# Optimization experiments

Measured on AMD Instinct MI355X. Metric: run time of the kernel, lower is better.

The kernel has to match this reference:

```python
import jax, jax.numpy as jnp
from jax import lax
import numpy as np

B, S = 128, 512
TARGET_SIZE = 32
T = TARGET_SIZE + 4  # tag_size, START = T-2, END = T-1


def setup_inputs() -> dict:
    key = jax.random.key(0)
    k1, k2, k3, k4 = jax.random.split(key, 4)
    feats = jax.random.normal(k1, (B, S, T), dtype=jnp.float32)
    # contiguous-prefix mask (lengths in [S//2, S])
    lengths = jax.random.randint(k2, (B,), S // 2, S + 1)
    mask = (jnp.arange(S)[None, :] < lengths[:, None]).astype(jnp.int32)
    tags = jax.random.randint(k3, (B, S), 0, TARGET_SIZE).astype(jnp.int32)
    # learned transitions, with the hard constraints from __init__
    transitions = 0.1 * jax.random.normal(k4, (T, T), dtype=jnp.float32)
    transitions = transitions.at[:, T - 2].set(-1000.0)  # nothing -> START
    transitions = transitions.at[T - 1, :].set(-1000.0)  # END -> nothing
    return {"feats": feats, "transitions": transitions, "mask": mask, "tags": tags}


def _nll(feats, transitions, mask, tags):
    # feats: (B,S,T), transitions: (T,T) with [i,j] = score(prev=i -> cur=j)
    b, s, t = feats.shape
    START, END = t - 2, t - 1
    fdtype = feats.dtype

    feats_t = jnp.swapaxes(feats, 0, 1)   # (S,B,T)
    mask_t = jnp.swapaxes(mask, 0, 1)     # (S,B)

    # ---- forward algorithm (partition function) ----
    # scores[t,b,i,j] = feats[b,t,j] + transitions[i,j]
    part0 = feats_t[0] + transitions[START][None, :]  # (B,T): alpha after step 0

    def step(part, xs):
        f_step, m_step = xs  # (B,T), (B,)
        # cur[b,i,j] = feats[b,j] + trans[i,j] + part[b,i]
        cur = f_step[:, None, :] + transitions[None, :, :] + part[:, :, None]
        new_part = jax.nn.logsumexp(cur, axis=1)  # (B,T)
        part = jnp.where(m_step[:, None].astype(bool), new_part, part)
        return part, None

    part, _ = lax.scan(step, part0, (feats_t[1:], mask_t[1:]))
    final = jax.nn.logsumexp(part[:, :, None] + transitions[None, :, :], axis=1)  # (B,T)
    forward_score = jnp.sum(final[:, END])

    # ---- gold score ----
    tags_i = tags.astype(jnp.int32)
    prev_tags = jnp.concatenate(
        [jnp.full((b, 1), START, dtype=jnp.int32), tags_i[:, :-1]], axis=1)  # (B,S)
    emit = jnp.take_along_axis(feats, tags_i[:, :, None], axis=2)[:, :, 0]    # (B,S)
    trans_sc = transitions[prev_tags, tags_i]                                  # (B,S)
    tg_energy = jnp.sum((emit + trans_sc) * mask.astype(fdtype))
    lengths = jnp.sum(mask, axis=1).astype(jnp.int32)                          # (B,)
    end_ids = jnp.take_along_axis(tags_i, (lengths - 1)[:, None], axis=1)[:, 0]
    end_energy = jnp.sum(transitions[end_ids, END])
    gold_score = tg_energy + end_energy

    # average_batch = True
    return (forward_score - gold_score) / jnp.asarray(b, fdtype)


def reference(feats, transitions, mask, tags):
    return _nll(feats, transitions, mask, tags)
```

## Files before the change

### kernel.cpp

```cpp
#include <hip/hip_runtime.h>


namespace {
constexpr int kB = 128;
constexpr int kS = 512;
constexpr int kT = 36;
constexpr int kStart = 34;
constexpr int kEnd = 35;

__device__ __forceinline__ float readlane_f(float v, int lane) {
    return __builtin_bit_cast(float, __builtin_amdgcn_readlane(__builtin_bit_cast(int, v), lane));
}

__device__ __forceinline__ float wave_sum(float v) {
#pragma unroll
    for (int off = 32; off; off >>= 1) v += __shfl_xor(v, off, 64);
    return v;
}
__device__ __forceinline__ int wave_sum_i(int v) {
#pragma unroll
    for (int off = 32; off; off >>= 1) v += __shfl_xor(v, off, 64);
    return v;
}

#define FOR34(X) \
    X(0, 0) X(1, 1) X(2, 2) X(3, 3) X(4, 0) X(5, 1) X(6, 2) X(7, 3) \
    X(8, 0) X(9, 1) X(10, 2) X(11, 3) X(12, 0) X(13, 1) X(14, 2) X(15, 3) \
    X(16, 0) X(17, 1) X(18, 2) X(19, 3) X(20, 0) X(21, 1) X(22, 2) X(23, 3) \
    X(24, 0) X(25, 1) X(26, 2) X(27, 3) X(28, 0) X(29, 1) X(30, 2) X(31, 3) \
    X(32, 0) X(33, 1)

#define FMDECL(n, a) float Fm##n;
#define FMINIT(n, a) Fm##n = __expf(trans[(n)*kT + jc]);
#define BMDECL(n, a) float Bm##n;
#define BMINIT(n, a) Bm##n = __expf(trans[jc * kT + (n)]);
#define FDOT(n, a) v##a = fmaf(readlane_f(q, n), Fm##n, v##a);
#define BDOT(n, a) w##a = fmaf(readlane_f(pp, n), Bm##n, w##a);

#define LDT(t) fl[(size_t)(((t) < 0) ? 0 : (((t) > kS - 1) ? (kS - 1) : (t))) * kT]

__global__ __attribute__((amdgpu_flat_work_group_size(512, 512)))
void crf_seg_kernel(const float* __restrict__ feats,
                    const float* __restrict__ trans,
                    const int* __restrict__ mask,
                    const int* __restrict__ tags,
                    float* __restrict__ out) {
    const int b = blockIdx.x;
    const int tid = threadIdx.x;
    const int wv = tid >> 6;
    const int j = tid & 63;
    const int jc = (j < kT) ? j : (kT - 1);
    const float* fbase = feats + (size_t)b * kS * kT;
    const float* fl = fbase + jc;
    const int* mb = mask + b * kS;
    const int* tb = tags + b * kS;

    __shared__ float vec[8][64];
    __shared__ float cc[8];

    int len = 0;
#pragma unroll
    for (int k = 0; k < kS / 64; ++k) len += mb[k * 64 + j];
    len = __builtin_amdgcn_readfirstlane(wave_sum_i(len));

    const int c = (len + 3) / 5;
    const int Gp = (c + 3) >> 2;

    float C = 0.f;

    if (wv < 4) {
        FOR34(FMDECL)
        FOR34(FMINIT)
        const int t0 = 1 + wv * c;
        const int cnt = c;
        float q;
        if (wv == 0) {
            const float a0 = (j < kT) ? (fl[0] + trans[kStart * kT + jc]) : -1e30f;
            C = readlane_f(a0, 0);
            q = __expf(a0 - C);
        } else {
            q = (jc == kStart) ? 0.f : 1.f;
        }

        auto fstep = [&](float ef, int s) {
            float v0 = 0.f, v1 = 0.f, v2 = 0.f, v3 = 0.f;
            FOR34(FDOT)
            const float nq = ((v0 + v1) + (v2 + v3)) * ef;
            q = (s < cnt) ? nq : q;
        };

        float p0, p1, p2, p3, e0, e1, e2, e3;
        p0 = LDT(t0 + 0); p1 = LDT(t0 + 1); p2 = LDT(t0 + 2); p3 = LDT(t0 + 3);
        e0 = __expf(p0); e1 = __expf(p1); e2 = __expf(p2); e3 = __expf(p3);
        p0 = LDT(t0 + 4); p1 = LDT(t0 + 5); p2 = LDT(t0 + 6); p3 = LDT(t0 + 7);

#pragma unroll 1
        for (int g = 0; g < Gp; ++g) {
            const int s = 4 * g;
            fstep(e0, s); fstep(e1, s + 1); fstep(e2, s + 2); fstep(e3, s + 3);
            e0 = __expf(p0); e1 = __expf(p1); e2 = __expf(p2); e3 = __expf(p3);
            p0 = LDT(t0 + s + 8);  p1 = LDT(t0 + s + 9);
            p2 = LDT(t0 + s + 10); p3 = LDT(t0 + s + 11);
            if (s + 4 < cnt) {
                const float mf = readlane_f(q, 0);
                C += __logf(mf);
                e0 *= __builtin_amdgcn_rcpf(mf);
            }
        }
        vec[wv][j] = q;
        if (j == 0) cc[wv] = C;
    } else {
        FOR34(BMDECL)
        FOR34(BMINIT)
        const bool real = (wv == 7);
        const int tau0 = real ? (len - 1) : ((wv - 2) * c);
        const int cnt = real ? (len - 1 - 4 * c) : c;
        float gg = real ? __expf(trans[jc * kT + kEnd])
                        : ((jc == kEnd) ? 0.f : 1.f);

        auto bstep = [&](float eb, int s) {
            const float pp = eb * gg;
            float w0 = 0.f, w1 = 0.f, w2 = 0.f, w3 = 0.f;
            FOR34(BDOT)
            const float ng = (w0 + w1) + (w2 + w3);
            gg = (s < cnt) ? ng : gg;
        };

        float p0, p1, p2, p3, e0, e1, e2, e3;
        p0 = LDT(tau0 - 0); p1 = LDT(tau0 - 1); p2 = LDT(tau0 - 2); p3 = LDT(tau0 - 3);
        e0 = __expf(p0); e1 = __expf(p1); e2 = __expf(p2); e3 = __expf(p3);
        p0 = LDT(tau0 - 4); p1 = LDT(tau0 - 5); p2 = LDT(tau0 - 6); p3 = LDT(tau0 - 7);

#pragma unroll 1
        for (int g = 0; g < Gp; ++g) {
            const int s = 4 * g;
            bstep(e0, s); bstep(e1, s + 1); bstep(e2, s + 2); bstep(e3, s + 3);
            e0 = __expf(p0); e1 = __expf(p1); e2 = __expf(p2); e3 = __expf(p3);
            p0 = LDT(tau0 - s - 8);  p1 = LDT(tau0 - s - 9);
            p2 = LDT(tau0 - s - 10); p3 = LDT(tau0 - s - 11);
            if (s + 4 < cnt) {
                const float mg = readlane_f(gg, 0);
                C += __logf(mg);
                e0 *= __builtin_amdgcn_rcpf(mg);
            }
        }
        vec[wv][j] = gg;
        if (j == 0) cc[wv] = C;
    }

    __syncthreads();

    if (wv == 0) {
        const float msk = (j < kT) ? 1.f : 0.f;
        const float d1 = wave_sum(msk * vec[4][j] * vec[0][j]);
        const float d2 = wave_sum(msk * vec[5][j] * vec[1][j]);
        const float d3 = wave_sum(msk * vec[6][j] * vec[2][j]);
        const float d4 = wave_sum(msk * vec[7][j] * vec[3][j]);
        const float n1 = wave_sum(msk * vec[1][j]);
        const float n2 = wave_sum(msk * vec[2][j]);
        const float n3 = wave_sum(msk * vec[3][j]);
        const float forward_b = cc[0] + cc[4] + cc[5] + cc[6] + cc[7]
            + __logf(d1) + __logf(d2) + __logf(d3) + __logf(d4)
            - __logf(n1) - __logf(n2) - __logf(n3);

        float gold = 0.f;
        for (int k = j; k < kS; k += 64) {
            if (k < len) {
                const int tg = tb[k];
                const int pv = (k == 0) ? kStart : tb[k - 1];
                gold += fbase[(size_t)k * kT + tg] + trans[pv * kT + tg];
            }
        }
        gold = wave_sum(gold);

        if (j == 0) {
            gold += trans[tb[len - 1] * kT + kEnd];
            atomicAdd(out, (forward_b - gold) * (1.0f / kB));
        }
    }
}

}

extern "C" void kernel_launch(void* const* d_in, const int* in_sizes, int n_in,
                              void* d_out, int out_size, void* d_ws, size_t ws_size,
                              hipStream_t stream) {
    const float* feats = (const float*)d_in[0];
    const float* trans = (const float*)d_in[1];
    const int* mask = (const int*)d_in[2];
    const int* tags = (const int*)d_in[3];
    float* out = (float*)d_out;

    (void)hipMemsetAsync(out, 0, sizeof(float), stream);
    crf_seg_kernel<<<dim3(kB), dim3(512), 0, stream>>>(feats, trans, mask, tags, out);
}
```

Before: 98.95 us.

## Split CRF chain segments into per-wave blocks and add combine kernel

New measurement: 93.88 us. 5.1% less time.

```diff
diff --git a/kernel.cpp b/kernel.cpp
--- a/kernel.cpp
+++ b/kernel.cpp
@@ -8,6 +8,9 @@
 constexpr int kStart = 34;
 constexpr int kEnd = 35;
 
+__device__ float g_vec[kB * 8][64];
+__device__ float g_cc[kB * 8];
+
 __device__ __forceinline__ float readlane_f(float v, int lane) {
     return __builtin_bit_cast(float, __builtin_amdgcn_readlane(__builtin_bit_cast(int, v), lane));
 }
@@ -39,30 +42,27 @@
 
 #define LDT(t) fl[(size_t)(((t) < 0) ? 0 : (((t) > kS - 1) ? (kS - 1) : (t))) * kT]
 
-__global__ __attribute__((amdgpu_flat_work_group_size(512, 512)))
-void crf_seg_kernel(const float* __restrict__ feats,
-                    const float* __restrict__ trans,
-                    const int* __restrict__ mask,
-                    const int* __restrict__ tags,
-                    float* __restrict__ out) {
-    const int b = blockIdx.x;
-    const int tid = threadIdx.x;
-    const int wv = tid >> 6;
-    const int j = tid & 63;
+__device__ __forceinline__ int seq_len(const int* mb, int j) {
+    int len = 0;
+#pragma unroll
+    for (int k = 0; k < kS / 64; ++k) len += mb[k * 64 + j];
+    return __builtin_amdgcn_readfirstlane(wave_sum_i(len));
+}
+
+__global__ __attribute__((amdgpu_flat_work_group_size(64, 64),
+                          amdgpu_waves_per_eu(1, 1)))
+void crf_chain_kernel(const float* __restrict__ feats,
+                      const float* __restrict__ trans,
+                      const int* __restrict__ mask) {
+    const int b = blockIdx.x >> 3;
+    const int wv = blockIdx.x & 7;
+    const int j = threadIdx.x;
     const int jc = (j < kT) ? j : (kT - 1);
     const float* fbase = feats + (size_t)b * kS * kT;
     const float* fl = fbase + jc;
     const int* mb = mask + b * kS;
-    const int* tb = tags + b * kS;
-
-    __shared__ float vec[8][64];
-    __shared__ float cc[8];
-
-    int len = 0;
-#pragma unroll
-    for (int k = 0; k < kS / 64; ++k) len += mb[k * 64 + j];
-    len = __builtin_amdgcn_readfirstlane(wave_sum_i(len));
-
+
+    const int len = seq_len(mb, j);
     const int c = (len + 3) / 5;
     const int Gp = (c + 3) >> 2;
 
@@ -107,8 +107,8 @@
                 e0 *= __builtin_amdgcn_rcpf(mf);
             }
         }
-        vec[wv][j] = q;
-        if (j == 0) cc[wv] = C;
+        g_vec[blockIdx.x][j] = q;
+        if (j == 0) g_cc[blockIdx.x] = C;
     } else {
         FOR34(BMDECL)
         FOR34(BMINIT)
@@ -144,39 +144,51 @@
                 e0 *= __builtin_amdgcn_rcpf(mg);
             }
         }
-        vec[wv][j] = gg;
-        if (j == 0) cc[wv] = C;
+        g_vec[blockIdx.x][j] = gg;
+        if (j == 0) g_cc[blockIdx.x] = C;
     }
-
-    __syncthreads();
-
-    if (wv == 0) {
-        const float msk = (j < kT) ? 1.f : 0.f;
-        const float d1 = wave_sum(msk * vec[4][j] * vec[0][j]);
-        const float d2 = wave_sum(msk * vec[5][j] * vec[1][j]);
-        const float d3 = wave_sum(msk * vec[6][j] * vec[2][j]);
-        const float d4 = wave_sum(msk * vec[7][j] * vec[3][j]);
-        const float n1 = wave_sum(msk * vec[1][j]);
-        const float n2 = wave_sum(msk * vec[2][j]);
-        const float n3 = wave_sum(msk * vec[3][j]);
-        const float forward_b = cc[0] + cc[4] + cc[5] + cc[6] + cc[7]
-            + __logf(d1) + __logf(d2) + __logf(d3) + __logf(d4)
-            - __logf(n1) - __logf(n2) - __logf(n3);
-
-        float gold = 0.f;
-        for (int k = j; k < kS; k += 64) {
-            if (k < len) {
-                const int tg = tb[k];
-                const int pv = (k == 0) ? kStart : tb[k - 1];
-                gold += fbase[(size_t)k * kT + tg] + trans[pv * kT + tg];
-            }
-        }
-        gold = wave_sum(gold);
-
-        if (j == 0) {
-            gold += trans[tb[len - 1] * kT + kEnd];
-            atomicAdd(out, (forward_b - gold) * (1.0f / kB));
-        }
+}
+
+__global__ __attribute__((amdgpu_flat_work_group_size(64, 64)))
+void crf_meet_kernel(const float* __restrict__ feats,
+                     const float* __restrict__ trans,
+                     const int* __restrict__ mask,
+                     const int* __restrict__ tags,
+                     float* __restrict__ out) {
+    const int b = blockIdx.x;
+    const int j = threadIdx.x;
+    const float* fbase = feats + (size_t)b * kS * kT;
+    const int* mb = mask + b * kS;
+    const int* tb = tags + b * kS;
+    const int len = seq_len(mb, j);
+    const int base = b * 8;
+
+    const float msk = (j < kT) ? 1.f : 0.f;
+    const float d1 = wave_sum(msk * g_vec[base + 4][j] * g_vec[base + 0][j]);
+    const float d2 = wave_sum(msk * g_vec[base + 5][j] * g_vec[base + 1][j]);
+    const float d3 = wave_sum(msk * g_vec[base + 6][j] * g_vec[base + 2][j]);
+    const float d4 = wave_sum(msk * g_vec[base + 7][j] * g_vec[base + 3][j]);
+    const float n1 = wave_sum(msk * g_vec[base + 1][j]);
+    const float n2 = wave_sum(msk * g_vec[base + 2][j]);
+    const float n3 = wave_sum(msk * g_vec[base + 3][j]);
+    const float forward_b = g_cc[base + 0] + g_cc[base + 4] + g_cc[base + 5]
+        + g_cc[base + 6] + g_cc[base + 7]
+        + __logf(d1) + __logf(d2) + __logf(d3) + __logf(d4)
+        - __logf(n1) - __logf(n2) - __logf(n3);
+
+    float gold = 0.f;
+    for (int k = j; k < kS; k += 64) {
+        if (k < len) {
+            const int tg = tb[k];
+            const int pv = (k == 0) ? kStart : tb[k - 1];
+            gold += fbase[(size_t)k * kT + tg] + trans[pv * kT + tg];
+        }
+    }
+    gold = wave_sum(gold);
+
+    if (j == 0) {
+        gold += trans[tb[len - 1] * kT + kEnd];
+        atomicAdd(out, (forward_b - gold) * (1.0f / kB));
     }
 }
 
@@ -192,5 +204,6 @@
     float* out = (float*)d_out;
 
     (void)hipMemsetAsync(out, 0, sizeof(float), stream);
-    crf_seg_kernel<<<dim3(kB), dim3(512), 0, stream>>>(feats, trans, mask, tags, out);
-}
+    crf_chain_kernel<<<dim3(kB * 8), dim3(64), 0, stream>>>(feats, trans, mask);
+    crf_meet_kernel<<<dim3(kB), dim3(64), 0, stream>>>(feats, trans, mask, tags, out);
+}
```

## Pair forward and backward CRF segments in each wave to halve block size

Applied to the files above, without the earlier changes.

New measurement: 101.5 us. 1.03x slower.

```diff
diff --git a/kernel.cpp b/kernel.cpp
--- a/kernel.cpp
+++ b/kernel.cpp
@@ -39,15 +39,23 @@
 
 #define LDT(t) fl[(size_t)(((t) < 0) ? 0 : (((t) > kS - 1) ? (kS - 1) : (t))) * kT]
 
-__global__ __attribute__((amdgpu_flat_work_group_size(512, 512)))
-void crf_seg_kernel(const float* __restrict__ feats,
-                    const float* __restrict__ trans,
-                    const int* __restrict__ mask,
-                    const int* __restrict__ tags,
-                    float* __restrict__ out) {
+__device__ __forceinline__ int seq_len(const int* mb, int j) {
+    int len = 0;
+#pragma unroll
+    for (int k = 0; k < kS / 64; ++k) len += mb[k * 64 + j];
+    return __builtin_amdgcn_readfirstlane(wave_sum_i(len));
+}
+
+__global__ __attribute__((amdgpu_flat_work_group_size(256, 256),
+                          amdgpu_waves_per_eu(1, 1)))
+void crf_pair_kernel(const float* __restrict__ feats,
+                     const float* __restrict__ trans,
+                     const int* __restrict__ mask,
+                     const int* __restrict__ tags,
+                     float* __restrict__ out) {
     const int b = blockIdx.x;
     const int tid = threadIdx.x;
-    const int wv = tid >> 6;
+    const int w = tid >> 6;
     const int j = tid & 63;
     const int jc = (j < kT) ? j : (kT - 1);
     const float* fbase = feats + (size_t)b * kS * kT;
@@ -55,111 +63,98 @@
     const int* mb = mask + b * kS;
     const int* tb = tags + b * kS;
 
-    __shared__ float vec[8][64];
-    __shared__ float cc[8];
+    __shared__ float xq[4][64];
+    __shared__ float xg[4][64];
+    __shared__ float cqb[4], cgb[4];
 
-    int len = 0;
-#pragma unroll
-    for (int k = 0; k < kS / 64; ++k) len += mb[k * 64 + j];
-    len = __builtin_amdgcn_readfirstlane(wave_sum_i(len));
-
+    const int len = seq_len(mb, j);
     const int c = (len + 3) / 5;
     const int Gp = (c + 3) >> 2;
 
-    float C = 0.f;
+    FOR34(FMDECL) FOR34(FMINIT)
+    FOR34(BMDECL) FOR34(BMINIT)
 
-    if (wv < 4) {
-        FOR34(FMDECL)
-        FOR34(FMINIT)
-        const int t0 = 1 + wv * c;
-        const int cnt = c;
-        float q;
-        if (wv == 0) {
-            const float a0 = (j < kT) ? (fl[0] + trans[kStart * kT + jc]) : -1e30f;
-            C = readlane_f(a0, 0);
-            q = __expf(a0 - C);
-        } else {
-            q = (jc == kStart) ? 0.f : 1.f;
-        }
+    const int t0f = 1 + w * c;
+    const int cntf = c;
+    float q, Cq = 0.f;
+    if (w == 0) {
+        const float a0 = (j < kT) ? (fl[0] + trans[kStart * kT + jc]) : -1e30f;
+        Cq = readlane_f(a0, 0);
+        q = __expf(a0 - Cq);
+    } else {
+        q = (jc == kStart) ? 0.f : 1.f;
+    }
 
-        auto fstep = [&](float ef, int s) {
-            float v0 = 0.f, v1 = 0.f, v2 = 0.f, v3 = 0.f;
-            FOR34(FDOT)
-            const float nq = ((v0 + v1) + (v2 + v3)) * ef;
-            q = (s < cnt) ? nq : q;
-        };
+    const bool real = (w == 0);
+    const int tau0 = real ? (len - 1) : ((w + 1) * c);
+    const int cntb = real ? (len - 1 - 4 * c) : c;
+    float gg = real ? __expf(trans[jc * kT + kEnd])
+                    : ((jc == kEnd) ? 0.f : 1.f);
+    float Cg = 0.f;
 
-        float p0, p1, p2, p3, e0, e1, e2, e3;
-        p0 = LDT(t0 + 0); p1 = LDT(t0 + 1); p2 = LDT(t0 + 2); p3 = LDT(t0 + 3);
-        e0 = __expf(p0); e1 = __expf(p1); e2 = __expf(p2); e3 = __expf(p3);
-        p0 = LDT(t0 + 4); p1 = LDT(t0 + 5); p2 = LDT(t0 + 6); p3 = LDT(t0 + 7);
+    auto fstep = [&](float ef, int s) {
+        float v0 = 0.f, v1 = 0.f, v2 = 0.f, v3 = 0.f;
+        FOR34(FDOT)
+        const float nq = ((v0 + v1) + (v2 + v3)) * ef;
+        q = (s < cntf) ? nq : q;
+    };
+    auto bstep = [&](float eb, int s) {
+        const float pp = eb * gg;
+        float w0 = 0.f, w1 = 0.f, w2 = 0.f, w3 = 0.f;
+        FOR34(BDOT)
+        const float ng = (w0 + w1) + (w2 + w3);
+        gg = (s < cntb) ? ng : gg;
+    };
+
+    float pf0, pf1, pf2, pf3, ef0, ef1, ef2, ef3;
+    float pb0, pb1, pb2, pb3, eb0, eb1, eb2, eb3;
+    pf0 = LDT(t0f + 0); pf1 = LDT(t0f + 1); pf2 = LDT(t0f + 2); pf3 = LDT(t0f + 3);
+    ef0 = __expf(pf0); ef1 = __expf(pf1); ef2 = __expf(pf2); ef3 = __expf(pf3);
+    pf0 = LDT(t0f + 4); pf1 = LDT(t0f + 5); pf2 = LDT(t0f + 6); pf3 = LDT(t0f + 7);
+    pb0 = LDT(tau0 - 0); pb1 = LDT(tau0 - 1); pb2 = LDT(tau0 - 2); pb3 = LDT(tau0 - 3);
+    eb0 = __expf(pb0); eb1 = __expf(pb1); eb2 = __expf(pb2); eb3 = __expf(pb3);
+    pb0 = LDT(tau0 - 4); pb1 = LDT(tau0 - 5); pb2 = LDT(tau0 - 6); pb3 = LDT(tau0 - 7);
 
 #pragma unroll 1
-        for (int g = 0; g < Gp; ++g) {
-            const int s = 4 * g;
-            fstep(e0, s); fstep(e1, s + 1); fstep(e2, s + 2); fstep(e3, s + 3);
-            e0 = __expf(p0); e1 = __expf(p1); e2 = __expf(p2); e3 = __expf(p3);
-            p0 = LDT(t0 + s + 8);  p1 = LDT(t0 + s + 9);
-            p2 = LDT(t0 + s + 10); p3 = LDT(t0 + s + 11);
-            if (s + 4 < cnt) {
-                const float mf = readlane_f(q, 0);
-                C += __logf(mf);
-                e0 *= __builtin_amdgcn_rcpf(mf);
-            }
+    for (int g = 0; g < Gp; ++g) {
+        const int s = 4 * g;
+        fstep(ef0, s);     bstep(eb0, s);
+        fstep(ef1, s + 1); bstep(eb1, s + 1);
+        fstep(ef2, s + 2); bstep(eb2, s + 2);
+        fstep(ef3, s + 3); bstep(eb3, s + 3);
+        ef0 = __expf(pf0); ef1 = __expf(pf1); ef2 = __expf(pf2); ef3 = __expf(pf3);
+        pf0 = LDT(t0f + s + 8);  pf1 = LDT(t0f + s + 9);
+        pf2 = LDT(t0f + s + 10); pf3 = LDT(t0f + s + 11);
+        eb0 = __expf(pb0); eb1 = __expf(pb1); eb2 = __expf(pb2); eb3 = __expf(pb3);
+        pb0 = LDT(tau0 - s - 8);  pb1 = LDT(tau0 - s - 9);
+        pb2 = LDT(tau0 - s - 10); pb3 = LDT(tau0 - s - 11);
+        if (s + 4 < cntf) {
+            const float mf = readlane_f(q, 0);
+            Cq += __logf(mf);
+            ef0 *= __builtin_amdgcn_rcpf(mf);
         }
-        vec[wv][j] = q;
-        if (j == 0) cc[wv] = C;
-    } else {
-        FOR34(BMDECL)
-        FOR34(BMINIT)
-        const bool real = (wv == 7);
-        const int tau0 = real ? (len - 1) : ((wv - 2) * c);
-        const int cnt = real ? (len - 1 - 4 * c) : c;
-        float gg = real ? __expf(trans[jc * kT + kEnd])
-                        : ((jc == kEnd) ? 0.f : 1.f);
-
-        auto bstep = [&](float eb, int s) {
-            const float pp = eb * gg;
-            float w0 = 0.f, w1 = 0.f, w2 = 0.f, w3 = 0.f;
-            FOR34(BDOT)
-            const float ng = (w0 + w1) + (w2 + w3);
-            gg = (s < cnt) ? ng : gg;
-        };
-
-        float p0, p1, p2, p3, e0, e1, e2, e3;
-        p0 = LDT(tau0 - 0); p1 = LDT(tau0 - 1); p2 = LDT(tau0 - 2); p3 = LDT(tau0 - 3);
-        e0 = __expf(p0); e1 = __expf(p1); e2 = __expf(p2); e3 = __expf(p3);
-        p0 = LDT(tau0 - 4); p1 = LDT(tau0 - 5); p2 = LDT(tau0 - 6); p3 = LDT(tau0 - 7);
-
-#pragma unroll 1
-        for (int g = 0; g < Gp; ++g) {
-            const int s = 4 * g;
-            bstep(e0, s); bstep(e1, s + 1); bstep(e2, s + 2); bstep(e3, s + 3);
-            e0 = __expf(p0); e1 = __expf(p1); e2 = __expf(p2); e3 = __expf(p3);
-            p0 = LDT(tau0 - s - 8);  p1 = LDT(tau0 - s - 9);
-            p2 = LDT(tau0 - s - 10); p3 = LDT(tau0 - s - 11);
-            if (s + 4 < cnt) {
-                const float mg = readlane_f(gg, 0);
-                C += __logf(mg);
-                e0 *= __builtin_amdgcn_rcpf(mg);
-            }
+        if (s + 4 < cntb) {
+            const float mg = readlane_f(gg, 0);
+            Cg += __logf(mg);
+            eb0 *= __builtin_amdgcn_rcpf(mg);
         }
-        vec[wv][j] = gg;
-        if (j == 0) cc[wv] = C;
     }
 
+    xq[w][j] = q;
+    xg[w][j] = gg;
+    if (j == 0) { cqb[w] = Cq; cgb[w] = Cg; }
     __syncthreads();
 
-    if (wv == 0) {
+    if (w == 0) {
         const float msk = (j < kT) ? 1.f : 0.f;
-        const float d1 = wave_sum(msk * vec[4][j] * vec[0][j]);
-        const float d2 = wave_sum(msk * vec[5][j] * vec[1][j]);
-        const float d3 = wave_sum(msk * vec[6][j] * vec[2][j]);
-        const float d4 = wave_sum(msk * vec[7][j] * vec[3][j]);
-        const float n1 = wave_sum(msk * vec[1][j]);
-        const float n2 = wave_sum(msk * vec[2][j]);
-        const float n3 = wave_sum(msk * vec[3][j]);
-        const float forward_b = cc[0] + cc[4] + cc[5] + cc[6] + cc[7]
+        const float d1 = wave_sum(msk * xg[1][j] * xq[0][j]);
+        const float d2 = wave_sum(msk * xg[2][j] * xq[1][j]);
+        const float d3 = wave_sum(msk * xg[3][j] * xq[2][j]);
+        const float d4 = wave_sum(msk * xg[0][j] * xq[3][j]);
+        const float n1 = wave_sum(msk * xq[1][j]);
+        const float n2 = wave_sum(msk * xq[2][j]);
+        const float n3 = wave_sum(msk * xq[3][j]);
+        const float forward_b = cqb[0] + cgb[1] + cgb[2] + cgb[3] + cgb[0]
             + __logf(d1) + __logf(d2) + __logf(d3) + __logf(d4)
             - __logf(n1) - __logf(n2) - __logf(n3);
 
@@ -192,5 +187,5 @@
     float* out = (float*)d_out;
 
     (void)hipMemsetAsync(out, 0, sizeof(float), stream);
-    crf_seg_kernel<<<dim3(kB), dim3(512), 0, stream>>>(feats, trans, mask, tags, out);
+    crf_pair_kernel<<<dim3(kB), dim3(256), 0, stream>>>(feats, trans, mask, tags, out);
 }
```
